# Kernel tuning notes

Measured on AMD Instinct MI355X. Metric: run time of the kernel, lower is better.

The kernel has to match this reference:

```python
import jax, jax.numpy as jnp
import numpy as np

DIM = 1024
HEADS = 16
DHEAD = 64
INNER = HEADS * DHEAD
EPS = 1e-5


def layer_norm(x, g, b):
    mu = jnp.mean(x, axis=-1, keepdims=True)
    var = jnp.mean(jnp.square(x - mu), axis=-1, keepdims=True)
    return (x - mu) * jax.lax.rsqrt(var + EPS) * g + b


def apply_rope(x, cos, sin):
    # x: [b, h, s, d]; cos/sin broadcast as [1, 1, s, d/2]
    d2 = x.shape[-1] // 2
    x1, x2 = x[..., :d2], x[..., d2:]
    return jnp.concatenate([x1 * cos - x2 * sin, x2 * cos + x1 * sin], axis=-1)


def setup_inputs() -> dict:
    key = jax.random.key(0)
    ks = jax.random.split(key, 10)
    B, N, S = 8, 256, 4096
    latents = jax.random.normal(ks[0], (B, N, DIM), dtype=jnp.float32)
    context = jax.random.normal(ks[1], (B, S, DIM), dtype=jnp.float32)
    cos = jax.random.uniform(ks[2], (S, DHEAD // 2), dtype=jnp.float32)
    sin = jax.random.uniform(ks[3], (S, DHEAD // 2), dtype=jnp.float32)
    init = lambda k, shp, fan_in: jax.random.normal(k, shp, dtype=jnp.float32) / np.sqrt(fan_in)
    return {
        "latents": latents,
        "context": context,
        "cos": cos,
        "sin": sin,
        "ln_lat_g": jnp.ones((DIM,), jnp.float32),
        "ln_lat_b": jnp.zeros((DIM,), jnp.float32),
        "ln_ctx_g": jnp.ones((DIM,), jnp.float32),
        "ln_ctx_b": jnp.zeros((DIM,), jnp.float32),
        "Wq": init(ks[4], (DIM, INNER), DIM),
        "Wkv": init(ks[5], (DIM, 2 * INNER), DIM),
        "Wo": init(ks[6], (INNER, DIM), INNER),
        "bo": jnp.zeros((DIM,), jnp.float32),
    }


def reference(latents, context, cos, sin, ln_lat_g, ln_lat_b, ln_ctx_g, ln_ctx_b, Wq, Wkv, Wo, bo):
    b, n, _ = latents.shape
    s = context.shape[1]
    lat = layer_norm(latents, ln_lat_g, ln_lat_b)
    ctx = layer_norm(context, ln_ctx_g, ln_ctx_b)
    q = (lat @ Wq).reshape(b, n, HEADS, DHEAD).transpose(0, 2, 1, 3)   # [b,h,n,d]
    kv = ctx @ Wkv
    k, v = jnp.split(kv, 2, axis=-1)
    k = k.reshape(b, s, HEADS, DHEAD).transpose(0, 2, 1, 3)           # [b,h,s,d]
    v = v.reshape(b, s, HEADS, DHEAD).transpose(0, 2, 1, 3)
    k = apply_rope(k, cos[None, None], sin[None, None])
    scale = DHEAD ** (-0.5)
    attn = jnp.einsum('bhnd,bhsd->bhns', q, k) * scale
    attn = jnp.clip(attn, -11.0, 11.0)
    attn = jax.nn.softmax(attn, axis=-1)
    out = jnp.einsum('bhns,bhsd->bhnd', attn, v)
    out = out.transpose(0, 2, 1, 3).reshape(b, n, INNER)
    return out @ Wo + bo
```

## Files before the change

### kernel.cpp

```cpp
#include <hip/hip_runtime.h>
#include <math.h>

#define DIM   1024
#define HEADS 16
#define DHEAD 64
#define NB    8
#define NLAT  256
#define SCTX  4096

typedef short bf16x8 __attribute__((ext_vector_type(8)));
typedef float f32x4  __attribute__((ext_vector_type(4)));

__device__ __forceinline__ unsigned short f2b(float f) {
    union { float f; unsigned u; } x; x.f = f;
    unsigned r = x.u + 0x7FFFu + ((x.u >> 16) & 1u);
    return (unsigned short)(r >> 16);
}

#define LN_BLOCKS (NB * NLAT + NB * SCTX)
__global__ __launch_bounds__(256) void prep_all(
    const float* __restrict__ latents, const float* __restrict__ context,
    const float* __restrict__ g_lat, const float* __restrict__ b_lat,
    const float* __restrict__ g_ctx, const float* __restrict__ b_ctx,
    const float* __restrict__ Wq, const float* __restrict__ Wkv,
    const float* __restrict__ Wo,
    unsigned short* __restrict__ lat_b, unsigned short* __restrict__ ctx_b,
    unsigned short* __restrict__ Wqb, unsigned short* __restrict__ Wkvb,
    unsigned short* __restrict__ Wob)
{
    __shared__ unsigned short tile[32][33];
    int gb = blockIdx.x, t = threadIdx.x;
    if (gb < LN_BLOCKS) {
        const float* x; const float* g; const float* b; unsigned short* y; int r;
        if (gb < NB * NLAT) { x = latents; g = g_lat; b = b_lat; y = lat_b; r = gb; }
        else { x = context; g = g_ctx; b = b_ctx; y = ctx_b; r = gb - NB * NLAT; }
        float* ls = (float*)tile;
        float* lq = ls + 4;
        float* st = ls + 8;
        float4 v = ((const float4*)(x + (size_t)r * DIM))[t];
        float s  = v.x + v.y + v.z + v.w;
        float sq = v.x * v.x + v.y * v.y + v.z * v.z + v.w * v.w;
        #pragma unroll
        for (int off = 32; off > 0; off >>= 1) {
            s  += __shfl_down(s, off);
            sq += __shfl_down(sq, off);
        }
        int wid = t >> 6, lane = t & 63;
        if (lane == 0) { ls[wid] = s; lq[wid] = sq; }
        __syncthreads();
        if (t == 0) {
            s  = ls[0] + ls[1] + ls[2] + ls[3];
            sq = lq[0] + lq[1] + lq[2] + lq[3];
            float m   = s * (1.0f / DIM);
            float var = sq * (1.0f / DIM) - m * m;
            st[0] = m;
            st[1] = rsqrtf(var + 1e-5f);
        }
        __syncthreads();
        float mu = st[0], rs = st[1];
        float4 gg = ((const float4*)g)[t];
        float4 bb = ((const float4*)b)[t];
        ushort4 o;
        o.x = f2b((v.x - mu) * rs * gg.x + bb.x);
        o.y = f2b((v.y - mu) * rs * gg.y + bb.y);
        o.z = f2b((v.z - mu) * rs * gg.z + bb.z);
        o.w = f2b((v.w - mu) * rs * gg.w + bb.w);
        ((ushort4*)(y + (size_t)r * DIM))[t] = o;
    } else {
        int id = gb - LN_BLOCKS;
        int z = id >> 10, y = (id >> 5) & 31, xb = id & 31;
        const float* W; unsigned short* Wt; int N, coloff = 0;
        switch (z) {
            case 0: W = Wq;  Wt = Wqb;  N = DIM;     break;
            case 1: W = Wkv; Wt = Wkvb; N = 2 * DIM; break;
            case 2: W = Wkv; Wt = Wkvb; N = 2 * DIM; coloff = DIM; break;
            default: W = Wo; Wt = Wob;  N = DIM;     break;
        }
        int n0 = xb * 32 + coloff, k0 = y * 32;
        int tx = t & 31, ty = t >> 5;
        #pragma unroll
        for (int i = 0; i < 4; ++i) {
            int k = k0 + ty + i * 8;
            tile[tx][ty + i * 8] = f2b(W[(size_t)k * N + n0 + tx]);
        }
        __syncthreads();
        #pragma unroll
        for (int i = 0; i < 4; ++i) {
            int n = n0 + ty + i * 8;
            Wt[(size_t)n * DIM + k0 + tx] = tile[ty + i * 8][tx];
        }
    }
}

__global__ __launch_bounds__(256, 2) void gemm_mfma(
    const unsigned short* __restrict__ A, const unsigned short* __restrict__ Bn,
    const unsigned short* __restrict__ Aq, const unsigned short* __restrict__ Bq,
    int K, const float* __restrict__ bias,
    const float* __restrict__ cosp, const float* __restrict__ sinp,
    float* __restrict__ outf,
    unsigned short* __restrict__ outk, unsigned short* __restrict__ outv,
    unsigned short* __restrict__ outq,
    int mode, int ldc)
{
    __shared__ __align__(16) unsigned short As[128 * 64];
    __shared__ __align__(16) unsigned short Bs[128 * 64];
    int t = threadIdx.x;
    int wave = t >> 6, lane = t & 63;
    int g = blockIdx.x;
    int m_tile, n_tile;
    if (mode == 2) {
        if (g >= 4096) {
            g -= 4096; mode = 1;
            A = Aq; Bn = Bq;
            n_tile = g & 7; m_tile = g >> 3;
        } else {
            int xcd = g & 7, j = g >> 3;
            n_tile = j & 15;
            m_tile = (xcd << 5) + (j >> 4);
        }
    } else {
        n_tile = g & 7; m_tile = g >> 3;
    }
    int m_base = m_tile * 128, n_base = n_tile * 128;
    int wr = wave >> 1, wc = wave & 1;
    int quad = lane >> 4, ln = lane & 15;

    f32x4 zero = {0.f, 0.f, 0.f, 0.f};
    f32x4 acc[4][4];
    #pragma unroll
    for (int i = 0; i < 4; ++i)
        #pragma unroll
        for (int j = 0; j < 4; ++j) acc[i][j] = zero;

    const unsigned short* Ag = A  + (size_t)m_base * K;
    const unsigned short* Bg = Bn + (size_t)n_base * K;

    int srow  = lane >> 3;
    int schk  = ((lane & 7) ^ srow) * 8;

    for (int k0 = 0; k0 < K; k0 += 64) {
        __syncthreads();
        #pragma unroll
        for (int j = 0; j < 4; ++j) {
            int grp = j * 4 + wave;
            int row = grp * 8 + srow;
            __builtin_amdgcn_global_load_lds(
                (const __attribute__((address_space(1))) void*)(Ag + (size_t)row * K + k0 + schk),
                (__attribute__((address_space(3))) void*)(As + grp * 512 + lane * 8),
                16, 0, 0);
            __builtin_amdgcn_global_load_lds(
                (const __attribute__((address_space(1))) void*)(Bg + (size_t)row * K + k0 + schk),
                (__attribute__((address_space(3))) void*)(Bs + grp * 512 + lane * 8),
                16, 0, 0);
        }
        __syncthreads();
        #pragma unroll
        for (int kk = 0; kk < 2; ++kk) {
            bf16x8 af[4], bfr[4];
            int slot = ((kk * 4 + quad) ^ (ln & 7)) * 8;
            #pragma unroll
            for (int i = 0; i < 4; ++i) {
                af[i]  = *(const bf16x8*)(As + (wr * 64 + i * 16 + ln) * 64 + slot);
                bfr[i] = *(const bf16x8*)(Bs + (wc * 64 + i * 16 + ln) * 64 + slot);
            }
            #pragma unroll
            for (int i = 0; i < 4; ++i)
                #pragma unroll
                for (int j = 0; j < 4; ++j)
                    acc[i][j] = __builtin_amdgcn_mfma_f32_16x16x32_bf16(af[i], bfr[j], acc[i][j], 0, 0, 0);
        }
    }

    int cl = ln, rq = quad;
    if (mode == 2 && n_base >= DIM) {
        #pragma unroll
        for (int i = 0; i < 4; ++i) {
            int s0 = m_base + wr * 64 + i * 16 + rq * 4;
            int b  = s0 >> 12, s = s0 & 4095;
            #pragma unroll
            for (int j = 0; j < 4; ++j) {
                int n2 = n_base + wc * 64 + j * 16 + cl - DIM;
                int h = n2 >> 6, d = n2 & 63;
                ushort4 pk;
                pk.x = f2b(acc[i][j][0]); pk.y = f2b(acc[i][j][1]);
                pk.z = f2b(acc[i][j][2]); pk.w = f2b(acc[i][j][3]);
                *(ushort4*)(outv + (((size_t)(b * HEADS + h) * DHEAD + d) * SCTX) + s) = pk;
            }
        }
    } else if (mode == 2) {
        #pragma unroll
        for (int i = 0; i < 4; ++i) {
            #pragma unroll
            for (int r = 0; r < 4; ++r) {
                int m = m_base + wr * 64 + i * 16 + rq * 4 + r;
                int b = m >> 12, s = m & 4095;
                #pragma unroll
                for (int j = 0; j < 2; ++j) {
                    int n = n_base + wc * 64 + j * 16 + cl;
                    int h = n >> 6, d1 = n & 63;
                    float x1 = acc[i][j][r], x2 = acc[i][j + 2][r];
                    float c  = cosp[s * 32 + d1];
                    float sn = sinp[s * 32 + d1];
                    unsigned short* kr =
                        outk + (((size_t)(b * HEADS + h) * SCTX + s) * DHEAD) + d1;
                    kr[0]  = f2b(x1 * c - x2 * sn);
                    kr[32] = f2b(x2 * c + x1 * sn);
                }
            }
        }
    } else {
        #pragma unroll
        for (int i = 0; i < 4; ++i) {
            #pragma unroll
            for (int j = 0; j < 4; ++j) {
                #pragma unroll
                for (int r = 0; r < 4; ++r) {
                    int m = m_base + wr * 64 + i * 16 + rq * 4 + r;
                    int n = n_base + wc * 64 + j * 16 + cl;
                    float cv = acc[i][j][r];
                    if (mode == 0) {
                        outf[(size_t)m * ldc + n] = cv + bias[n];
                    } else {
                        int b = m >> 8, nn = m & 255;
                        int h = n >> 6, d = n & 63;
                        outq[(((size_t)(b * HEADS + h) * NLAT + nn) * DHEAD) + d] = f2b(cv);
                    }
                }
            }
        }
    }
}

__global__ __launch_bounds__(256, 2) void attn_mfma(
    const unsigned short* __restrict__ qb,
    const unsigned short* __restrict__ kb,
    const unsigned short* __restrict__ vtb,
    float* __restrict__ accp,
    float* __restrict__ lp)
{
    __shared__ __align__(16) unsigned short Ks[64 * 64];
    __shared__ __align__(16) unsigned short Vs[64 * 64];
    __shared__ __align__(16) unsigned short Ps[4 * 32 * 72];

    int t = threadIdx.x, w = t >> 6, l = t & 63;
    int bh = blockIdx.x >> 3;
    int qh = (blockIdx.x >> 2) & 1;
    int sh = blockIdx.x & 3;
    int quad = l >> 4, ln = l & 15;
    int q0 = qh * 128 + w * 32;

    bf16x8 qf[2][2];
    const unsigned short* qbase = qb + ((size_t)bh * NLAT + q0) * DHEAD;
    #pragma unroll
    for (int qsub = 0; qsub < 2; ++qsub)
        #pragma unroll
        for (int kc = 0; kc < 2; ++kc)
            qf[qsub][kc] = *(const bf16x8*)(qbase + (qsub * 16 + ln) * DHEAD + kc * 32 + quad * 8);

    f32x4 acc[2][4];
    #pragma unroll
    for (int i = 0; i < 2; ++i)
        #pragma unroll
        for (int j = 0; j < 4; ++j) acc[i][j] = (f32x4){0.f, 0.f, 0.f, 0.f};
    float lacc[2] = {0.f, 0.f};

    int srow = t >> 3;
    int schk = t & 7;
    const unsigned short* kgb = kb  + (size_t)bh * SCTX * DHEAD;
    const unsigned short* vgb = vtb + (size_t)bh * DHEAD * SCTX;
    unsigned short* Pw = Ps + w * 32 * 72;

    const int s_begin = sh * 1024;
    const int NT = 1024 / 64;

    uint4 kreg[2], vreg[2];
    #pragma unroll
    for (int i = 0; i < 2; ++i) {
        int row = srow + 32 * i;
        kreg[i] = *(const uint4*)(kgb + (size_t)(s_begin + row) * DHEAD + schk * 8);
        vreg[i] = *(const uint4*)(vgb + (size_t)row * SCTX + s_begin + schk * 8);
    }

    for (int it = 0; it < NT; ++it) {
        __syncthreads();
        #pragma unroll
        for (int i = 0; i < 2; ++i) {
            int row = srow + 32 * i;
            int cpos = schk ^ (row & 7);
            *(uint4*)(Ks + row * 64 + cpos * 8) = kreg[i];
            *(uint4*)(Vs + row * 64 + cpos * 8) = vreg[i];
        }
        __syncthreads();
        if (it + 1 < NT) {
            int s0n = s_begin + (it + 1) * 64;
            #pragma unroll
            for (int i = 0; i < 2; ++i) {
                int row = srow + 32 * i;
                kreg[i] = *(const uint4*)(kgb + (size_t)(s0n + row) * DHEAD + schk * 8);
                vreg[i] = *(const uint4*)(vgb + (size_t)row * SCTX + s0n + schk * 8);
            }
        }

        #pragma unroll
        for (int msub = 0; msub < 4; ++msub) {
            bf16x8 af[2];
            #pragma unroll
            for (int kc = 0; kc < 2; ++kc) {
                int sr = msub * 16 + ln;
                int ck = (4 * kc + quad) ^ (ln & 7);
                af[kc] = *(const bf16x8*)(Ks + sr * 64 + ck * 8);
            }
            #pragma unroll
            for (int nsub = 0; nsub < 2; ++nsub) {
                f32x4 c = {0.f, 0.f, 0.f, 0.f};
                c = __builtin_amdgcn_mfma_f32_16x16x32_bf16(af[0], qf[nsub][0], c, 0, 0, 0);
                c = __builtin_amdgcn_mfma_f32_16x16x32_bf16(af[1], qf[nsub][1], c, 0, 0, 0);
                ushort4 pk;
                #pragma unroll
                for (int r = 0; r < 4; ++r) {
                    float sc = fminf(fmaxf(c[r] * 0.125f, -11.f), 11.f);
                    float p  = __expf(sc - 11.f);
                    lacc[nsub] += p;
                    ((unsigned short*)&pk)[r] = f2b(p);
                }
                *(ushort4*)(Pw + (nsub * 16 + ln) * 72 + msub * 16 + quad * 4) = pk;
            }
        }
        #pragma unroll
        for (int kc = 0; kc < 2; ++kc) {
            bf16x8 pa[2];
            #pragma unroll
            for (int qsub = 0; qsub < 2; ++qsub)
                pa[qsub] = *(const bf16x8*)(Pw + (qsub * 16 + ln) * 72 + kc * 32 + quad * 8);
            #pragma unroll
            for (int dsub = 0; dsub < 4; ++dsub) {
                int dr = dsub * 16 + ln;
                int ck = (4 * kc + quad) ^ (ln & 7);
                bf16x8 vb = *(const bf16x8*)(Vs + dr * 64 + ck * 8);
                acc[0][dsub] = __builtin_amdgcn_mfma_f32_16x16x32_bf16(pa[0], vb, acc[0][dsub], 0, 0, 0);
                acc[1][dsub] = __builtin_amdgcn_mfma_f32_16x16x32_bf16(pa[1], vb, acc[1][dsub], 0, 0, 0);
            }
        }
    }

    float* accs = accp + (size_t)sh * (NB * HEADS * NLAT * DHEAD);
    float* ls   = lp   + (size_t)sh * (NB * HEADS * NLAT);

    #pragma unroll
    for (int nsub = 0; nsub < 2; ++nsub) {
        float v = lacc[nsub];
        v += __shfl_xor(v, 16);
        v += __shfl_xor(v, 32);
        if (l < 16)
            ls[bh * NLAT + q0 + nsub * 16 + l] = v;
    }
    #pragma unroll
    for (int qsub = 0; qsub < 2; ++qsub)
        #pragma unroll
        for (int dsub = 0; dsub < 4; ++dsub)
            #pragma unroll
            for (int r = 0; r < 4; ++r) {
                int qg = q0 + qsub * 16 + quad * 4 + r;
                int dg = dsub * 16 + ln;
                accs[((size_t)bh * NLAT + qg) * DHEAD + dg] = acc[qsub][dsub][r];
            }
}

__global__ __launch_bounds__(256) void attn_finalize(
    const float* __restrict__ accp, const float* __restrict__ lp,
    unsigned short* __restrict__ aob)
{
    const int ACC = NB * HEADS * NLAT * DHEAD;
    const int LSZ = NB * HEADS * NLAT;
    int idx = blockIdx.x * 256 + threadIdx.x;
    int d = idx & 63;
    int rest = idx >> 6;
    int n = rest & 255, bh = rest >> 8;
    int b = bh >> 4, h = bh & 15;
    float a = accp[idx] + accp[idx + ACC] + accp[idx + 2 * ACC] + accp[idx + 3 * ACC];
    float l = lp[rest] + lp[rest + LSZ] + lp[rest + 2 * LSZ] + lp[rest + 3 * LSZ];
    aob[(((size_t)b * NLAT + n) * HEADS + h) * DHEAD + d] = f2b(a / l);
}

extern "C" void kernel_launch(void* const* d_in, const int* in_sizes, int n_in,
                              void* d_out, int out_size, void* d_ws, size_t ws_size,
                              hipStream_t stream) {
    const float* latents  = (const float*)d_in[0];
    const float* context  = (const float*)d_in[1];
    const float* cosp     = (const float*)d_in[2];
    const float* sinp     = (const float*)d_in[3];
    const float* ln_lat_g = (const float*)d_in[4];
    const float* ln_lat_b = (const float*)d_in[5];
    const float* ln_ctx_g = (const float*)d_in[6];
    const float* ln_ctx_b = (const float*)d_in[7];
    const float* Wq  = (const float*)d_in[8];
    const float* Wkv = (const float*)d_in[9];
    const float* Wo  = (const float*)d_in[10];
    const float* bo  = (const float*)d_in[11];
    float* out = (float*)d_out;

    char* base = (char*)d_ws;
    unsigned short* lat_b = (unsigned short*)(base + 0);
    unsigned short* ctx_b = (unsigned short*)(base + 4194304);
    unsigned short* Wqb   = (unsigned short*)(base + 71303168);
    unsigned short* Wkvb  = (unsigned short*)(base + 73400320);
    unsigned short* Wob   = (unsigned short*)(base + 77594624);
    unsigned short* q_b   = (unsigned short*)(base + 79691776);
    unsigned short* k_b   = (unsigned short*)(base + 83886080);
    unsigned short* vT_b  = (unsigned short*)(base + 150994944);
    float*          accp  = (float*)(base + 218103808);
    float*          lp    = (float*)(base + 251658240);
    unsigned short* aob   = (unsigned short*)(base + 252182528);

    hipLaunchKernelGGL(prep_all, dim3(LN_BLOCKS + 4096), dim3(256), 0, stream,
                       latents, context, ln_lat_g, ln_lat_b, ln_ctx_g, ln_ctx_b,
                       Wq, Wkv, Wo, lat_b, ctx_b, Wqb, Wkvb, Wob);
    hipLaunchKernelGGL(gemm_mfma, dim3(4096 + 128), dim3(256), 0, stream,
                       ctx_b, Wkvb, lat_b, Wqb, DIM, (const float*)nullptr,
                       cosp, sinp,
                       (float*)nullptr, k_b, vT_b, q_b, 2, 0);
    hipLaunchKernelGGL(attn_mfma, dim3(NB * HEADS * 8), dim3(256), 0, stream,
                       q_b, k_b, vT_b, accp, lp);
    hipLaunchKernelGGL(attn_finalize, dim3(NB * HEADS * NLAT * DHEAD / 256), dim3(256), 0, stream,
                       accp, lp, aob);
    hipLaunchKernelGGL(gemm_mfma, dim3(128), dim3(256), 0, stream,
                       aob, Wob, (const unsigned short*)nullptr, (const unsigned short*)nullptr,
                       DIM, bo,
                       (const float*)nullptr, (const float*)nullptr,
                       out, (unsigned short*)nullptr, (unsigned short*)nullptr,
                       (unsigned short*)nullptr, 0, DIM);
}
```

Before: 522.0 us.

## Double-buffer K/V shared tiles, fold softmax scale into Q, pack bf16 conversions

Attention K/V shared-memory tiles become double-buffered. The next tile is written to the alternate buffer after the compute, so each iteration needs one barrier instead of two. The 1/sqrt(d) scale is folded into the Q projection epilogue, which removes a multiply per score. P conversion uses the packed bf16x2 intrinsic. Shared memory grows by 16KB per block, which may reduce occupancy at 2 blocks per CU, and bf16 rounding of the pre-scaled Q shifts numerics slightly.

```diff
diff --git a/kernel.cpp b/kernel.cpp
--- a/kernel.cpp
+++ b/kernel.cpp
@@ -1,4 +1,5 @@
 #include <hip/hip_runtime.h>
+#include <hip/hip_bf16.h>
 #include <math.h>
 
 #define DIM   1024
@@ -15,6 +16,13 @@
     union { float f; unsigned u; } x; x.f = f;
     unsigned r = x.u + 0x7FFFu + ((x.u >> 16) & 1u);
     return (unsigned short)(r >> 16);
+}
+
+__device__ __forceinline__ unsigned pkbf16(float a, float b) {
+    float2 f2; f2.x = a; f2.y = b;
+    __hip_bfloat162 h = __float22bfloat162_rn(f2);
+    union { __hip_bfloat162 h; unsigned u; } cv; cv.h = h;
+    return cv.u;
 }
 
 #define LN_BLOCKS (NB * NLAT + NB * SCTX)
@@ -223,7 +231,8 @@
                     } else {
                         int b = m >> 8, nn = m & 255;
                         int h = n >> 6, d = n & 63;
-                        outq[(((size_t)(b * HEADS + h) * NLAT + nn) * DHEAD) + d] = f2b(cv);
+                        outq[(((size_t)(b * HEADS + h) * NLAT + nn) * DHEAD) + d] =
+                            f2b(cv * 0.125f);
                     }
                 }
             }
@@ -238,8 +247,8 @@
     float* __restrict__ accp,
     float* __restrict__ lp)
 {
-    __shared__ __align__(16) unsigned short Ks[64 * 64];
-    __shared__ __align__(16) unsigned short Vs[64 * 64];
+    __shared__ __align__(16) unsigned short Ks[2][64 * 64];
+    __shared__ __align__(16) unsigned short Vs[2][64 * 64];
     __shared__ __align__(16) unsigned short Ps[4 * 32 * 72];
 
     int t = threadIdx.x, w = t >> 6, l = t & 63;
@@ -266,6 +275,7 @@
 
     int srow = t >> 3;
     int schk = t & 7;
+    int cpos = schk ^ (srow & 7);
     const unsigned short* kgb = kb  + (size_t)bh * SCTX * DHEAD;
     const unsigned short* vgb = vtb + (size_t)bh * DHEAD * SCTX;
     unsigned short* Pw = Ps + w * 32 * 72;
@@ -280,17 +290,15 @@
         kreg[i] = *(const uint4*)(kgb + (size_t)(s_begin + row) * DHEAD + schk * 8);
         vreg[i] = *(const uint4*)(vgb + (size_t)row * SCTX + s_begin + schk * 8);
     }
+    #pragma unroll
+    for (int i = 0; i < 2; ++i) {
+        int row = srow + 32 * i;
+        *(uint4*)(&Ks[0][row * 64 + cpos * 8]) = kreg[i];
+        *(uint4*)(&Vs[0][row * 64 + cpos * 8]) = vreg[i];
+    }
 
     for (int it = 0; it < NT; ++it) {
-        __syncthreads();
-        #pragma unroll
-        for (int i = 0; i < 2; ++i) {
-            int row = srow + 32 * i;
-            int cpos = schk ^ (row & 7);
-            *(uint4*)(Ks + row * 64 + cpos * 8) = kreg[i];
-            *(uint4*)(Vs + row * 64 + cpos * 8) = vreg[i];
-        }
-        __syncthreads();
+        int buf = it & 1;
         if (it + 1 < NT) {
             int s0n = s_begin + (it + 1) * 64;
             #pragma unroll
@@ -300,6 +308,7 @@
                 vreg[i] = *(const uint4*)(vgb + (size_t)row * SCTX + s0n + schk * 8);
             }
         }
+        __syncthreads();
 
         #pragma unroll
         for (int msub = 0; msub < 4; ++msub) {
@@ -308,22 +317,24 @@
             for (int kc = 0; kc < 2; ++kc) {
                 int sr = msub * 16 + ln;
                 int ck = (4 * kc + quad) ^ (ln & 7);
-                af[kc] = *(const bf16x8*)(Ks + sr * 64 + ck * 8);
+                af[kc] = *(const bf16x8*)(&Ks[buf][sr * 64 + ck * 8]);
             }
             #pragma unroll
             for (int nsub = 0; nsub < 2; ++nsub) {
                 f32x4 c = {0.f, 0.f, 0.f, 0.f};
                 c = __builtin_amdgcn_mfma_f32_16x16x32_bf16(af[0], qf[nsub][0], c, 0, 0, 0);
                 c = __builtin_amdgcn_mfma_f32_16x16x32_bf16(af[1], qf[nsub][1], c, 0, 0, 0);
-                ushort4 pk;
+                float p[4];
                 #pragma unroll
                 for (int r = 0; r < 4; ++r) {
-                    float sc = fminf(fmaxf(c[r] * 0.125f, -11.f), 11.f);
-                    float p  = __expf(sc - 11.f);
-                    lacc[nsub] += p;
-                    ((unsigned short*)&pk)[r] = f2b(p);
+                    float sc = fminf(fmaxf(c[r], -11.f), 11.f);
+                    p[r] = __expf(sc - 11.f);
+                    lacc[nsub] += p[r];
                 }
-                *(ushort4*)(Pw + (nsub * 16 + ln) * 72 + msub * 16 + quad * 4) = pk;
+                uint2 pk;
+                pk.x = pkbf16(p[0], p[1]);
+                pk.y = pkbf16(p[2], p[3]);
+                *(uint2*)(Pw + (nsub * 16 + ln) * 72 + msub * 16 + quad * 4) = pk;
             }
         }
         #pragma unroll
@@ -336,9 +347,17 @@
             for (int dsub = 0; dsub < 4; ++dsub) {
                 int dr = dsub * 16 + ln;
                 int ck = (4 * kc + quad) ^ (ln & 7);
-                bf16x8 vb = *(const bf16x8*)(Vs + dr * 64 + ck * 8);
+                bf16x8 vb = *(const bf16x8*)(&Vs[buf][dr * 64 + ck * 8]);
                 acc[0][dsub] = __builtin_amdgcn_mfma_f32_16x16x32_bf16(pa[0], vb, acc[0][dsub], 0, 0, 0);
                 acc[1][dsub] = __builtin_amdgcn_mfma_f32_16x16x32_bf16(pa[1], vb, acc[1][dsub], 0, 0, 0);
+            }
+        }
+        if (it + 1 < NT) {
+            #pragma unroll
+            for (int i = 0; i < 2; ++i) {
+                int row = srow + 32 * i;
+                *(uint4*)(&Ks[buf ^ 1][row * 64 + cpos * 8]) = kreg[i];
+                *(uint4*)(&Vs[buf ^ 1][row * 64 + cpos * 8]) = vreg[i];
             }
         }
     }
```

Measured after the change: 514.6 us. About the same (-1.4%).
